# Performance work log

Measured on AMD Instinct MI355X. Metric: run time of the kernel, lower is better.

The kernel has to match this reference:

```python
import jax, jax.numpy as jnp
import numpy as np
from jax import lax

A_NUM = 3
STRIDES = (4, 8, 16, 32, 64)
LEVEL_HW = ((128, 208), (64, 104), (32, 52), (16, 26), (8, 13))
IMG_H, IMG_W = 512.0, 832.0
PRE_NMS, POST_NMS, NMS_TH = 6000, 1000, 0.7


def _base_anchors(base_size, ratios=(0.5, 1.0, 2.0), scales=(8.0,)):
    ratios = np.asarray(ratios, np.float64)
    scales = np.asarray(scales, np.float64)
    cx = cy = (base_size - 1) / 2.0
    size = float(base_size) * float(base_size)
    ws = np.round(np.sqrt(size / ratios))
    hs = np.round(ws * ratios)
    ws = (ws[:, None] * scales[None, :]).reshape(-1)
    hs = (hs[:, None] * scales[None, :]).reshape(-1)
    return np.stack([cx - 0.5 * (ws - 1), cy - 0.5 * (hs - 1),
                     cx + 0.5 * (ws - 1), cy + 0.5 * (hs - 1)], axis=1)


def _all_anchors():
    # generate_anchors_global: per-level shifted grids, concatenated, order (h, w, a)
    out = []
    for stride, (h, w) in zip(STRIDES, LEVEL_HW):
        base = _base_anchors(stride)  # [A,4]
        sx = np.arange(w) * stride
        sy = np.arange(h) * stride
        sx, sy = np.meshgrid(sx, sy)
        shifts = np.stack([sx.ravel(), sy.ravel(), sx.ravel(), sy.ravel()], axis=1)
        anc = (shifts[:, None, :] + base[None, :, :]).reshape(-1, 4)  # [H*W*A,4]
        out.append(anc)
    return np.concatenate(out, axis=0).astype(np.float32)

_ANCHORS = _all_anchors()


def _conv(x, w, b, pad):
    y = lax.conv_general_dilated(x, w, (1, 1), [(pad, pad), (pad, pad)],
                                 dimension_numbers=('NCHW', 'OIHW', 'NCHW'))
    return y + b[None, :, None, None]


def _bbox_transform_inv(anchors, deltas):
    w = anchors[:, 2] - anchors[:, 0] + 1.0
    h = anchors[:, 3] - anchors[:, 1] + 1.0
    cx = anchors[:, 0] + 0.5 * w
    cy = anchors[:, 1] + 0.5 * h
    dx, dy, dw, dh = deltas[:, 0], deltas[:, 1], deltas[:, 2], deltas[:, 3]
    pcx = dx * w + cx
    pcy = dy * h + cy
    pw = jnp.exp(dw) * w
    ph = jnp.exp(dh) * h
    return jnp.stack([pcx - 0.5 * pw, pcy - 0.5 * ph,
                      pcx + 0.5 * pw, pcy + 0.5 * ph], axis=1)


def _iou_one_to_many(box, boxes):
    area = (boxes[:, 2] - boxes[:, 0] + 1.0) * (boxes[:, 3] - boxes[:, 1] + 1.0)
    area_b = (box[2] - box[0] + 1.0) * (box[3] - box[1] + 1.0)
    xx1 = jnp.maximum(box[0], boxes[:, 0])
    yy1 = jnp.maximum(box[1], boxes[:, 1])
    xx2 = jnp.minimum(box[2], boxes[:, 2])
    yy2 = jnp.minimum(box[3], boxes[:, 3])
    iw = jnp.maximum(0.0, xx2 - xx1 + 1.0)
    ih = jnp.maximum(0.0, yy2 - yy1 + 1.0)
    inter = iw * ih
    return inter / (area + area_b - inter)


def _nms_fixed(boxes, scores, thresh, max_out):
    # greedy NMS with a fixed number of iterations (jit-friendly)
    def body(s, _):
        i = jnp.argmax(s)
        valid = s[i] > -jnp.inf
        ious = _iou_one_to_many(boxes[i], boxes)
        s2 = jnp.where(ious > thresh, -jnp.inf, s)
        s2 = s2.at[i].set(-jnp.inf)
        return s2, (i, valid)
    _, (idx, valid) = lax.scan(body, scores, None, length=max_out)
    return idx, valid


def _rpn_forward(feats, im_info, rpn_conv_w, rpn_conv_b, rpn_score_w,
                 rpn_score_b, rpn_bbox_w, rpn_bbox_b):
    fg_scores, bbox_deltas = [], []
    for p in feats:
        H, W = p.shape[-2], p.shape[-1]
        f = _conv(p, rpn_conv_w, rpn_conv_b, 1)              # [1,512,H,W]
        cls = _conv(f, rpn_score_w, rpn_score_b, 0)          # [1,2A,H,W]
        # _reshape_layer(.,2) + softmax(dim=1) + _reshape_layer back + permute
        prob = jax.nn.softmax(cls.reshape(1, 2, A_NUM, H, W), axis=1)
        prob = prob.reshape(1, 2 * A_NUM, H, W).transpose(0, 2, 3, 1)  # [1,H,W,2A]
        fg = prob[..., A_NUM:].reshape(-1)                    # fg prob, order (h,w,a)
        bb = _conv(f, rpn_bbox_w, rpn_bbox_b, 0).transpose(0, 2, 3, 1).reshape(-1, 4)
        fg_scores.append(fg)
        bbox_deltas.append(bb)
    scores = jnp.concatenate(fg_scores, axis=0)              # [Ntot]
    deltas = jnp.concatenate(bbox_deltas, axis=0)            # [Ntot,4]
    anchors = jnp.asarray(_ANCHORS)

    proposals = _bbox_transform_inv(anchors, deltas)
    # clip to image
    proposals = jnp.stack([
        jnp.clip(proposals[:, 0], 0.0, im_info[1] - 1.0),
        jnp.clip(proposals[:, 1], 0.0, im_info[0] - 1.0),
        jnp.clip(proposals[:, 2], 0.0, im_info[1] - 1.0),
        jnp.clip(proposals[:, 3], 0.0, im_info[0] - 1.0)], axis=1)

    # pre-NMS top-k by score
    top_scores, order = lax.top_k(scores, PRE_NMS)
    top_boxes = proposals[order]
    keep, valid = _nms_fixed(top_boxes, top_scores, NMS_TH, POST_NMS)
    vmask = valid.astype(top_boxes.dtype)[:, None]
    sel_boxes = top_boxes[keep] * vmask
    sel_scores = top_scores[keep][:, None] * vmask
    rois = jnp.concatenate([jnp.zeros((POST_NMS, 1), sel_boxes.dtype), sel_boxes], axis=1)
    return jnp.concatenate([rois, sel_scores], axis=1)        # [POST_NMS, 6]


def setup_inputs() -> dict:
    key = jax.random.key(0)
    ks = jax.random.split(key, 12)
    chans = 256
    feats = {}
    for i, (name, (h, w)) in enumerate(zip(['p2', 'p3', 'p4', 'p5', 'p6'], LEVEL_HW)):
        feats[name] = jax.random.normal(ks[i], (1, chans, h, w), jnp.float32)
    inp = dict(feats)
    inp['im_info'] = jnp.array([IMG_H, IMG_W, 1.0], jnp.float32)
    inp['rpn_conv_w'] = jax.random.normal(ks[5], (512, chans, 3, 3), jnp.float32) * 0.03
    inp['rpn_conv_b'] = jnp.zeros((512,), jnp.float32)
    inp['rpn_score_w'] = jax.random.normal(ks[6], (2 * A_NUM, 512, 1, 1), jnp.float32) * 0.03
    inp['rpn_score_b'] = jnp.zeros((2 * A_NUM,), jnp.float32)
    inp['rpn_bbox_w'] = jax.random.normal(ks[7], (4 * A_NUM, 512, 1, 1), jnp.float32) * 0.01
    inp['rpn_bbox_b'] = jnp.zeros((4 * A_NUM,), jnp.float32)
    return inp


def reference(p2, p3, p4, p5, p6, im_info, rpn_conv_w, rpn_conv_b,
              rpn_score_w, rpn_score_b, rpn_bbox_w, rpn_bbox_b):
    return _rpn_forward([p2, p3, p4, p5, p6], im_info, rpn_conv_w, rpn_conv_b,
                        rpn_score_w, rpn_score_b, rpn_bbox_w, rpn_bbox_b)
```

## Files before the change

### kernel.cpp

```cpp
#include <hip/hip_runtime.h>
#include <stdint.h>

#define N_ANCH   106392
#define PRE_NMS  6000
#define POST_NMS 1000
#define POOL_CAP 8192
#define NMS_BLKS 94
#define SUP_W    96

static __device__ const int    LV_H[5]      = {128, 64, 32, 16, 8};
static __device__ const int    LV_W[5]      = {208, 104, 52, 26, 13};
static __device__ const int    LV_STRIDE[5] = {4, 8, 16, 32, 64};
static __device__ const int    LV_PIX[5]    = {26624, 6656, 1664, 416, 104};
static __device__ const int    LV_TILE0[6]  = {0, 416, 520, 546, 553, 555};
static __device__ const int    LV_AOFF[6]   = {0, 79872, 99840, 104832, 106080, 106392};
static __device__ const int    GPOFF[6]     = {0, 26624, 33280, 34944, 35360, 35464};
static __device__ const double BASE_ANCH[5][3][4] = {
  {{-22.,-10.,25.,13.},   {-14.,-14.,17.,17.},    {-10.,-22.,13.,25.}},
  {{-40.,-20.,47.,27.},   {-28.,-28.,35.,35.},    {-20.,-44.,27.,51.}},
  {{-84.,-40.,99.,55.},   {-56.,-56.,71.,71.},    {-36.,-80.,51.,95.}},
  {{-164.,-72.,195.,103.},{-112.,-112.,143.,143.},{-76.,-168.,107.,199.}},
  {{-332.,-152.,395.,215.},{-224.,-224.,287.,287.},{-148.,-328.,211.,391.}}
};

__device__ __forceinline__ uint32_t sort32f(float f) {
  uint32_t u = __float_as_uint(f);
  return ((int)u < 0) ? ~u : (u | 0x80000000u);
}
__device__ __forceinline__ uint64_t sort64(double d) {
  uint64_t u = (uint64_t)__double_as_longlong(d);
  return ((long long)u < 0) ? ~u : (u | 0x8000000000000000ull);
}

__device__ __forceinline__ double combf(const float* sw, const float* bw, int c, int j) {
  if (j < 3) return (double)sw[(3 + j) * 512 + c] - (double)sw[j * 512 + c];
  return (double)bw[(j - 3) * 512 + c];
}

__global__ __launch_bounds__(256) void k_weff_part(const float* __restrict__ cw,
                                                   const float* __restrict__ sw,
                                                   const float* __restrict__ bw,
                                                   double* __restrict__ Wpart) {
  int chunk = blockIdx.x / 9;
  int tb = blockIdx.x % 9;
  int t = tb * 256 + threadIdx.x;
  int c0 = chunk * 32;
  double acc[15];
#pragma unroll
  for (int j = 0; j < 15; ++j) acc[j] = 0.0;
#pragma unroll 1
  for (int c = c0; c < c0 + 32; ++c) {
    double v = (double)cw[c * 2304 + t];
#pragma unroll
    for (int j = 0; j < 15; ++j) acc[j] += v * combf(sw, bw, c, j);
  }
  double* o = Wpart + (((size_t)chunk * 2304 + t) << 4);
#pragma unroll
  for (int j = 0; j < 15; ++j) o[j] = acc[j];
  o[15] = 0.0;
}

__global__ __launch_bounds__(256) void k_weff_fin(const double* __restrict__ Wpart,
                                                  const float* __restrict__ cb,
                                                  const float* __restrict__ sb,
                                                  const float* __restrict__ bb,
                                                  const float* __restrict__ sw,
                                                  const float* __restrict__ bw,
                                                  double* __restrict__ Weff,
                                                  double* __restrict__ fb,
                                                  float4* __restrict__ w3,
                                                  float* __restrict__ fb32) {
  if (blockIdx.x == 9) {
    __shared__ double ps[15][16];
    int tid = threadIdx.x;
    if (tid < 240) {
      int j = tid >> 4, part = tid & 15;
      double s = 0.0;
      for (int c = part * 32; c < part * 32 + 32; ++c)
        s += (double)cb[c] * combf(sw, bw, c, j);
      ps[j][part] = s;
    }
    __syncthreads();
    if (tid < 15) {
      double s = 0.0;
#pragma unroll
      for (int part = 0; part < 16; ++part) s += ps[tid][part];
      s += (tid < 3) ? ((double)sb[3 + tid] - (double)sb[tid]) : (double)bb[tid - 3];
      fb[tid] = s;
      if (tid < 3) fb32[tid] = (float)s;
    }
    if (tid == 15) fb32[3] = 0.f;
    return;
  }
  int t = blockIdx.x * 256 + threadIdx.x;
  double acc[15];
#pragma unroll
  for (int j = 0; j < 15; ++j) acc[j] = 0.0;
#pragma unroll 1
  for (int chunk = 0; chunk < 16; ++chunk) {
    const double* p = Wpart + (((size_t)chunk * 2304 + t) << 4);
#pragma unroll
    for (int j = 0; j < 15; ++j) acc[j] += p[j];
  }
  double* o = Weff + ((size_t)t << 4);
#pragma unroll
  for (int j = 0; j < 15; ++j) o[j] = acc[j];
  o[15] = 0.0;
  float4 wf;
  wf.x = (float)acc[0]; wf.y = (float)acc[1]; wf.z = (float)acc[2]; wf.w = 0.f;
  w3[t] = wf;
}

__global__ __launch_bounds__(256) void k_w5(const double* __restrict__ Weff,
                                            double* __restrict__ w5) {
  int idx = blockIdx.x * 256 + threadIdx.x;
  if (idx >= 2304 * 3) return;
  int t = idx / 3, a = idx % 3;
  int ci = t / 9, t9 = t % 9;
  const double* src = Weff + ((size_t)t << 4);
  double* dst = w5 + (size_t)ci * 192 + (size_t)(t9 * 3 + a) * 6;
  int jd = 3 + 4 * a;
  dst[0] = src[jd + 0];
  dst[1] = src[jd + 1];
  dst[2] = src[jd + 2];
  dst[3] = src[jd + 3];
  dst[4] = src[a];
  dst[5] = 0.0;
}

__device__ __forceinline__ void load9(float v[9], const float* __restrict__ ib,
                                      const bool rok[3], const bool cok[3],
                                      const int roff[3]) {
#pragma unroll
  for (int ky = 0; ky < 3; ++ky)
#pragma unroll
    for (int kx = 0; kx < 3; ++kx)
      v[ky * 3 + kx] = (rok[ky] && cok[kx]) ? ib[roff[ky] + kx] : 0.0f;
}

__global__ __launch_bounds__(256) void k_fast(
    const float* __restrict__ p0, const float* __restrict__ p1,
    const float* __restrict__ p2, const float* __restrict__ p3,
    const float* __restrict__ p4,
    const float4* __restrict__ w3, const float* __restrict__ fb32,
    float* __restrict__ logits32, uint32_t* __restrict__ hist) {
  __shared__ float4 w3s[2304];
  __shared__ float red[4][64][3];
  int tid = threadIdx.x, wv = tid >> 6, ln = tid & 63;
  for (int i = tid; i < 2304; i += 256) w3s[i] = w3[i];
  int t = blockIdx.x;
  int L = 0;
  while (L < 4 && t >= LV_TILE0[L + 1]) ++L;
  const float* inL = (L == 0) ? p0 : (L == 1) ? p1 : (L == 2) ? p2 : (L == 3) ? p3 : p4;
  int H = LV_H[L], W = LV_W[L], HW = H * W, PIX = LV_PIX[L];
  int pix = (t - LV_TILE0[L]) * 64 + ln;
  bool valid = pix < PIX;
  if (!valid) pix = PIX - 1;
  int h = pix / W, w = pix % W;
  bool rok[3], cok[3];
  int roff[3];
#pragma unroll
  for (int ky = 0; ky < 3; ++ky) {
    int iy = h + ky - 1;
    rok[ky] = (iy >= 0 && iy < H);
    roff[ky] = iy * W + w - 1;
  }
#pragma unroll
  for (int kx = 0; kx < 3; ++kx) {
    int ix = w + kx - 1;
    cok[kx] = (ix >= 0 && ix < W);
  }
  __syncthreads();
  float a0 = 0.f, a1 = 0.f, a2 = 0.f;
  int ci0 = wv * 64;
  const float* ib = inL + ci0 * HW;
#pragma unroll 1
  for (int ci = ci0; ci < ci0 + 64; ++ci, ib += HW) {
    float v[9];
    load9(v, ib, rok, cok, roff);
    const float4* wr = w3s + ci * 9;
#pragma unroll
    for (int t9 = 0; t9 < 9; ++t9) {
      float4 wt = wr[t9];
      float vv = v[t9];
      a0 += vv * wt.x; a1 += vv * wt.y; a2 += vv * wt.z;
    }
  }
  red[wv][ln][0] = a0; red[wv][ln][1] = a1; red[wv][ln][2] = a2;
  __syncthreads();
  if (wv == 0 && valid) {
    int gbase = LV_AOFF[L] + pix * 3;
#pragma unroll
    for (int a = 0; a < 3; ++a) {
      float f = (red[0][ln][a] + red[1][ln][a]) + (red[2][ln][a] + red[3][ln][a]);
      f += fb32[a];
      logits32[gbase + a] = f;
      atomicAdd(&hist[sort32f(f) >> 16], 1u);
    }
  }
}

__global__ __launch_bounds__(1024) void k_edge(const uint32_t* __restrict__ hist,
                                               uint32_t* __restrict__ cnts) {
  __shared__ uint32_t cs[1024];
  __shared__ uint32_t g_grp, g_suf;
  int t = threadIdx.x, wv = t >> 6, ln = t & 63;
#pragma unroll 4
  for (int r = 0; r < 64; ++r) {
    int g = r * 16 + wv;
    uint32_t x = hist[g * 64 + ln];
#pragma unroll
    for (int off = 32; off > 0; off >>= 1) x += __shfl_down(x, off);
    if (ln == 0) cs[g] = x;
  }
  __syncthreads();
  for (int off = 1; off < 1024; off <<= 1) {
    uint32_t v = cs[t] + ((t + off < 1024) ? cs[t + off] : 0u);
    __syncthreads();
    cs[t] = v;
    __syncthreads();
  }
  uint32_t sufnext = (t < 1023) ? cs[t + 1] : 0u;
  if (cs[t] >= PRE_NMS && sufnext < PRE_NMS) {
    g_grp = (uint32_t)t;
    g_suf = sufnext;
  }
  __syncthreads();
  if (t < 64) {
    uint32_t grp = g_grp, suf = g_suf;
    uint32_t x = hist[grp * 64 + t];
    uint32_t S = x;
#pragma unroll
    for (int off = 1; off < 64; off <<= 1) {
      uint32_t y = __shfl_down(S, off);
      if (t + off < 64) S += y;
    }
    unsigned long long mask = __ballot(suf + S >= PRE_NMS);
    int hi = 63 - (int)__clzll(mask);
    if (t == hi) {
      uint32_t e = grp * 64 + (uint32_t)hi;
      cnts[1] = (e > 2) ? e - 2 : 0;
    }
  }
}

__global__ __launch_bounds__(256) void k_cnt(const float* __restrict__ logits32,
                                             const uint32_t* __restrict__ cnts,
                                             uint32_t* __restrict__ bcnt) {
  __shared__ uint32_t wc[4];
  int tid = threadIdx.x;
  int i = blockIdx.x * 256 + tid;
  uint32_t edge = cnts[1];
  bool pass = (i < N_ANCH) && ((sort32f(logits32[i]) >> 16) >= edge);
  unsigned long long m = __ballot(pass);
  if ((tid & 63) == 0) wc[tid >> 6] = (uint32_t)__popcll(m);
  __syncthreads();
  if (tid == 0) bcnt[blockIdx.x] = wc[0] + wc[1] + wc[2] + wc[3];
}

__global__ __launch_bounds__(256) void k_fill(const float* __restrict__ logits32,
                                              uint32_t* __restrict__ cnts,
                                              const uint32_t* __restrict__ bcnt,
                                              uint32_t* __restrict__ alist) {
  __shared__ uint32_t red[256];
  __shared__ uint32_t woff[4];
  int tid = threadIdx.x, wv = tid >> 6, ln = tid & 63;
  uint32_t s = 0;
  for (int k = tid; k < blockIdx.x; k += 256) s += bcnt[k];
  red[tid] = s;
  __syncthreads();
#pragma unroll
  for (int off = 128; off > 0; off >>= 1) {
    if (tid < off) red[tid] += red[tid + off];
    __syncthreads();
  }
  uint32_t base = red[0];
  int i = blockIdx.x * 256 + tid;
  uint32_t edge = cnts[1];
  bool pass = (i < N_ANCH) && ((sort32f(logits32[i]) >> 16) >= edge);
  unsigned long long m = __ballot(pass);
  if (ln == 0) woff[wv] = (uint32_t)__popcll(m);
  __syncthreads();
  uint32_t off_in_blk = 0;
  for (int k = 0; k < wv; ++k) off_in_blk += woff[k];
  if (pass) {
    uint32_t pos = base + off_in_blk + (uint32_t)__popcll(m & ((1ull << ln) - 1ull));
    if (pos < POOL_CAP) alist[pos] = (uint32_t)i;
  }
  if (blockIdx.x == ((N_ANCH + 255) / 256 - 1) && tid == 0)
    cnts[0] = base + woff[0] + woff[1] + woff[2] + woff[3];
}

__global__ __launch_bounds__(256) void k_refine(
    const float* __restrict__ p0, const float* __restrict__ p1,
    const float* __restrict__ p2, const float* __restrict__ p3,
    const float* __restrict__ p4,
    const double* __restrict__ w5, const double* __restrict__ fb,
    const uint32_t* __restrict__ alist, const uint32_t* __restrict__ cnts,
    double* __restrict__ logits, double* __restrict__ deltas,
    uint64_t* __restrict__ pkey) {
  __shared__ int4 wlds[4][768];
  __shared__ double red[4][64][5];
  int tid = threadIdx.x, wv = tid >> 6, ln = tid & 63;
  int cnt = (int)cnts[0];
  if (cnt > POOL_CAP) cnt = POOL_CAP;
  int base = blockIdx.x * 64;
  if (base >= cnt) return;
  int slot = base + ln;
  if (slot >= cnt) slot = cnt - 1;
  int gi = (int)alist[slot];
  int gpix = gi / 3, a = gi - gpix * 3;
  int L = 0;
  while (L < 4 && gpix >= GPOFF[L + 1]) ++L;
  int pix = gpix - GPOFF[L];
  const float* inL = (L == 0) ? p0 : (L == 1) ? p1 : (L == 2) ? p2 : (L == 3) ? p3 : p4;
  int H = LV_H[L], W = LV_W[L], HW = H * W;
  int h = pix / W, w = pix % W;
  bool rok[3], cok[3];
  int roff[3];
#pragma unroll
  for (int ky = 0; ky < 3; ++ky) {
    int iy = h + ky - 1;
    rok[ky] = (iy >= 0 && iy < H);
    roff[ky] = iy * W + w - 1;
  }
#pragma unroll
  for (int kx = 0; kx < 3; ++kx) {
    int ix = w + kx - 1;
    cok[kx] = (ix >= 0 && ix < W);
  }
  const char* wbc = (const char*)&wlds[wv][0];
  {
    const int4* gs = (const int4*)((const char*)w5 + (size_t)(wv * 64) * 1536);
    int4 r[12];
#pragma unroll
    for (int i = 0; i < 12; ++i) r[i] = gs[i * 64 + ln];
#pragma unroll
    for (int i = 0; i < 12; ++i) wlds[wv][i * 64 + ln] = r[i];
  }
  double sc = 0.0, d0 = 0.0, d1 = 0.0, d2 = 0.0, d3 = 0.0;
  const float* ibn = inL + (size_t)(wv * 64) * HW;
  float vn[9];
  load9(vn, ibn, rok, cok, roff);
#pragma unroll 1
  for (int k = 0; k < 8; ++k) {
    int4 r[12];
    if (k < 7) {
      const int4* gs =
          (const int4*)((const char*)w5 + (size_t)(wv * 64 + (k + 1) * 8) * 1536);
#pragma unroll
      for (int i = 0; i < 12; ++i) r[i] = gs[i * 64 + ln];
    }
#pragma unroll 1
    for (int c2 = 0; c2 < 8; ++c2) {
      float vc[9];
#pragma unroll
      for (int q = 0; q < 9; ++q) vc[q] = vn[q];
      int lc = k * 8 + c2;
      if (lc < 63) {
        ibn += HW;
        load9(vn, ibn, rok, cok, roff);
      }
      const char* b2 = wbc + c2 * 1536 + a * 48;
#pragma unroll
      for (int t9 = 0; t9 < 9; ++t9) {
        double vd = (double)vc[t9];
        double2 w01 = *(const double2*)(b2 + t9 * 144);
        double2 w23 = *(const double2*)(b2 + t9 * 144 + 16);
        double  w4  = *(const double*)(b2 + t9 * 144 + 32);
        d0 += vd * w01.x; d1 += vd * w01.y;
        d2 += vd * w23.x; d3 += vd * w23.y;
        sc += vd * w4;
      }
    }
    if (k < 7) {
#pragma unroll
      for (int i = 0; i < 12; ++i) wlds[wv][i * 64 + ln] = r[i];
    }
  }
  red[wv][ln][0] = sc;
  red[wv][ln][1] = d0; red[wv][ln][2] = d1;
  red[wv][ln][3] = d2; red[wv][ln][4] = d3;
  __syncthreads();
  if (wv == 0) {
    int js = a, jd = 3 + 4 * a;
    double f[5];
#pragma unroll
    for (int j = 0; j < 5; ++j)
      f[j] = red[0][ln][j] + red[1][ln][j] + red[2][ln][j] + red[3][ln][j];
    double lg = f[0] + fb[js];
    logits[gi] = lg;
    deltas[gi * 4 + 0] = f[1] + fb[jd + 0];
    deltas[gi * 4 + 1] = f[2] + fb[jd + 1];
    deltas[gi * 4 + 2] = f[3] + fb[jd + 2];
    deltas[gi * 4 + 3] = f[4] + fb[jd + 3];
    pkey[slot] = (sort64(lg) & ~0x1FFFFull) | (uint64_t)(0x1FFFFu - (uint32_t)gi);
  }
}

__global__ __launch_bounds__(256) void k_rank_cnt(const uint32_t* __restrict__ cnts,
                                                  const uint64_t* __restrict__ pkey,
                                                  uint32_t* __restrict__ rank32) {
  __shared__ uint64_t lk[512];
  int t = threadIdx.x;
  int cnt = (int)cnts[0];
  if (cnt > POOL_CAP) cnt = POOL_CAP;
  int it = blockIdx.x >> 4, jc = blockIdx.x & 15;
  int e = it * 256 + t;
  int c0 = jc * 512;
  if (it * 256 >= cnt || c0 >= cnt) return;
  int lim = cnt - c0; if (lim > 512) lim = 512;
  for (int i = t; i < 512; i += 256) lk[i] = (i < lim) ? pkey[c0 + i] : 0ull;
  __syncthreads();
  bool active = e < cnt;
  uint64_t mykey = active ? pkey[e] : ~0ull;
  int r = 0;
#pragma unroll 8
  for (int j = 0; j < 512; ++j) r += (lk[j] > mykey) ? 1 : 0;
  if (active && r) atomicAdd(&rank32[e], (uint32_t)r);
}

__global__ __launch_bounds__(256) void k_scatter(const uint32_t* __restrict__ cnts,
                                                 const uint64_t* __restrict__ pkey,
                                                 const uint32_t* __restrict__ rank32,
                                                 const double* __restrict__ logits,
                                                 const double* __restrict__ deltas,
                                                 const float* __restrict__ im_info,
                                                 double* __restrict__ ss,
                                                 double* __restrict__ sbx,
                                                 float4* __restrict__ bxf,
                                                 float* __restrict__ areaf) {
  int t = threadIdx.x;
  int cnt = (int)cnts[0];
  if (cnt > POOL_CAP) cnt = POOL_CAP;
  int e = blockIdx.x * 256 + t;
  if (blockIdx.x * 256 >= cnt) return;
  if (e >= cnt) return;
  int rank = (int)rank32[e];
  if (rank >= PRE_NMS) return;
  uint64_t mykey = pkey[e];
  int gi = 0x1FFFF - (int)(mykey & 0x1FFFFull);
  int L = 0;
  while (L < 4 && gi >= LV_AOFF[L + 1]) ++L;
  int rel = gi - LV_AOFF[L];
  int pix = rel / 3, a = rel % 3;
  int W = LV_W[L];
  int h = pix / W, w = pix % W;
  double imW1 = (double)im_info[1] - 1.0;
  double imH1 = (double)im_info[0] - 1.0;
  double shx = (double)(w * LV_STRIDE[L]), shy = (double)(h * LV_STRIDE[L]);
  double ax1 = BASE_ANCH[L][a][0] + shx, ay1 = BASE_ANCH[L][a][1] + shy;
  double ax2 = BASE_ANCH[L][a][2] + shx, ay2 = BASE_ANCH[L][a][3] + shy;
  double dx = deltas[gi * 4 + 0], dy = deltas[gi * 4 + 1];
  double dw = deltas[gi * 4 + 2], dh = deltas[gi * 4 + 3];
  double wa = ax2 - ax1 + 1.0, ha = ay2 - ay1 + 1.0;
  double cx = ax1 + 0.5 * wa, cy = ay1 + 0.5 * ha;
  double pcx = dx * wa + cx, pcy = dy * ha + cy;
  double pw = exp(dw) * wa, ph = exp(dh) * ha;
  double x1 = fmin(fmax(pcx - 0.5 * pw, 0.0), imW1);
  double y1 = fmin(fmax(pcy - 0.5 * ph, 0.0), imH1);
  double x2 = fmin(fmax(pcx + 0.5 * pw, 0.0), imW1);
  double y2 = fmin(fmax(pcy + 0.5 * ph, 0.0), imH1);
  ss[rank] = 1.0 / (1.0 + exp(-logits[gi]));
  sbx[rank * 4 + 0] = x1; sbx[rank * 4 + 1] = y1;
  sbx[rank * 4 + 2] = x2; sbx[rank * 4 + 3] = y2;
  float4 bf;
  bf.x = (float)x1; bf.y = (float)y1; bf.z = (float)x2; bf.w = (float)y2;
  bxf[rank] = bf;
  areaf[rank] = (float)((x2 - x1 + 1.0) * (y2 - y1 + 1.0));
}

__device__ __forceinline__ bool iou_gt(const double* A, const double* B) {
  double areaA = (A[2] - A[0] + 1.0) * (A[3] - A[1] + 1.0);
  double areaB = (B[2] - B[0] + 1.0) * (B[3] - B[1] + 1.0);
  double xx1 = fmax(A[0], B[0]), yy1 = fmax(A[1], B[1]);
  double xx2 = fmin(A[2], B[2]), yy2 = fmin(A[3], B[3]);
  double iw = fmax(0.0, xx2 - xx1 + 1.0), ih = fmax(0.0, yy2 - yy1 + 1.0);
  double inter = iw * ih;
  return inter > 0.7 * (areaA + areaB - inter);
}

__global__ __launch_bounds__(256) void k_build(const double* __restrict__ sbx,
                                               const float4* __restrict__ bxf,
                                               const float* __restrict__ areaf,
                                               uint64_t* __restrict__ Sup) {
  __shared__ float cbx[256][5];
  __shared__ float rbx[64][5];
  int blk = blockIdx.x;
  int rtile = blk / 24, ctile = blk % 24;
  int t = threadIdx.x, q = t >> 6, ln = t & 63;
  int r = rtile * 64 + ln;
  int w = ctile * 4 + q;
  {
    int c = ctile * 256 + t;
    float4 b;
    float ar;
    if (c < NMS_BLKS * 64) { b = bxf[c]; ar = areaf[c]; }
    else { b.x = b.y = b.z = b.w = 0.f; ar = 0.f; }
    cbx[t][0] = b.x; cbx[t][1] = b.y; cbx[t][2] = b.z; cbx[t][3] = b.w; cbx[t][4] = ar;
    if (t < 64) {
      int rr = rtile * 64 + t;
      float4 rb = bxf[rr];
      rbx[t][0] = rb.x; rbx[t][1] = rb.y; rbx[t][2] = rb.z; rbx[t][3] = rb.w;
      rbx[t][4] = areaf[rr];
    }
  }
  __syncthreads();
  uint64_t bits = 0ull;
  int j0 = w * 64;
  if (w < NMS_BLKS && j0 + 63 > r) {
    float ax1 = rbx[ln][0], ay1 = rbx[ln][1], ax2 = rbx[ln][2], ay2 = rbx[ln][3];
    float aar = rbx[ln][4];
#pragma unroll 4
    for (int jj = 0; jj < 64; ++jj) {
      int j = j0 + jj;
      if (j <= r) continue;
      int cl = q * 64 + jj;
      float iw = fminf(ax2, cbx[cl][2]) - fmaxf(ax1, cbx[cl][0]) + 1.f;
      float ih = fminf(ay2, cbx[cl][3]) - fmaxf(ay1, cbx[cl][1]) + 1.f;
      float inter = fmaxf(iw, 0.f) * fmaxf(ih, 0.f);
      float d = inter - 0.7f * (aar + cbx[cl][4] - inter);
      bool sup;
      if (d > 4.0f) sup = true;
      else if (d < -4.0f) sup = false;
      else sup = iou_gt(sbx + (size_t)r * 4, sbx + (size_t)j * 4);
      if (sup) bits |= 1ull << jj;
    }
  }
  Sup[(size_t)r * SUP_W + w] = bits;
}

__global__ __launch_bounds__(1024) void k_scan(const uint64_t* __restrict__ Sup,
                                               const double* __restrict__ ss,
                                               const double* __restrict__ sbx,
                                               float* __restrict__ out) {
  __shared__ uint16_t keep[POST_NMS];
  __shared__ uint32_t ext_arr[SUP_W][2];
  __shared__ int s_kcnt, s_done;
  __shared__ int s_pend[2][2];
  int t = threadIdx.x, wv = t >> 6, ln = t & 63;
  for (int i = t; i < SUP_W * 2; i += 1024) ext_arr[i >> 1][i & 1] = 0u;
  if (t == 0) { s_kcnt = 0; s_done = 0; }
  if (t < 4) s_pend[t >> 1][t & 1] = 0;
  uint64_t diag = 0ull, nxt = 0ull;
  if (wv == 0) {
    size_t r = (size_t)ln * SUP_W;
    diag = Sup[r + 0];
    nxt  = Sup[r + 1];
  }
  __syncthreads();
  for (int b = 0; b < NMS_BLKS; ++b) {
    if (wv == 0) {
      uint64_t myrow = diag & ~((2ull << ln) - 1ull);
      uint64_t mynxt = nxt;
      if (b + 1 < NMS_BLKS) {
        size_t r = (size_t)((b + 1) * 64 + ln) * SUP_W;
        diag = Sup[r + (b + 1)];
        nxt  = Sup[r + (b + 2)];
      }
      uint64_t ext = ((uint64_t)ext_arr[b][1] << 32) | ext_arr[b][0];
      int base = b * 64;
      if (base + 63 >= PRE_NMS) {
        int v = PRE_NMS - base;
        ext |= ~((1ull << v) - 1ull);
      }
      int K0 = s_kcnt;
      uint64_t avail;
      {
        uint64_t a0 = ~ext;
        uint32_t alo = __builtin_amdgcn_readfirstlane((uint32_t)a0);
        uint32_t ahi = __builtin_amdgcn_readfirstlane((uint32_t)(a0 >> 32));
        avail = ((uint64_t)ahi << 32) | alo;
      }
      uint32_t mr_lo = (uint32_t)myrow, mr_hi = (uint32_t)(myrow >> 32);
      uint32_t mn_lo = (uint32_t)mynxt, mn_hi = (uint32_t)(mynxt >> 32);
      uint64_t kp = 0ull, extn = 0ull;
      int lim = POST_NMS - K0, nk = 0;
      while (avail && nk < lim) {
        int i2 = __ffsll((unsigned long long)avail) - 1;
        uint32_t rlo = (uint32_t)__builtin_amdgcn_readlane((int)mr_lo, i2);
        uint32_t rhi = (uint32_t)__builtin_amdgcn_readlane((int)mr_hi, i2);
        uint32_t qlo = (uint32_t)__builtin_amdgcn_readlane((int)mn_lo, i2);
        uint32_t qhi = (uint32_t)__builtin_amdgcn_readlane((int)mn_hi, i2);
        kp |= 1ull << i2;
        ++nk;
        extn |= ((uint64_t)qhi << 32) | qlo;
        avail &= ~(((uint64_t)rhi << 32) | rlo);
        avail &= ~(1ull << i2);
      }
      if ((kp >> ln) & 1ull) {
        int pos = K0 + __popcll(kp & ((1ull << ln) - 1ull));
        keep[pos] = (uint16_t)(base + ln);
      }
      if (ln == 0) {
        if ((uint32_t)extn)         atomicOr(&ext_arr[b + 1][0], (uint32_t)extn);
        if ((uint32_t)(extn >> 32)) atomicOr(&ext_arr[b + 1][1],
                                             (uint32_t)(extn >> 32));
        s_kcnt = K0 + nk;
        s_pend[(b + 1) & 1][0] = K0;
        s_pend[(b + 1) & 1][1] = K0 + nk;
        if (K0 + nk >= POST_NMS || b + 1 >= NMS_BLKS) s_done = 1;
      }
    } else {
      int lo = s_pend[b & 1][0], hi = s_pend[b & 1][1];
      if (hi > lo) {
        int tt = t - 64;
        int g = tt / 96, w = tt - g * 96;
        if (w >= b + 1) {
          uint64_t v = 0ull;
          for (int q = lo + g; q < hi; q += 10)
            v |= Sup[(size_t)keep[q] * SUP_W + w];
          if (v) {
            if ((uint32_t)v)         atomicOr(&ext_arr[w][0], (uint32_t)v);
            if ((uint32_t)(v >> 32)) atomicOr(&ext_arr[w][1], (uint32_t)(v >> 32));
          }
        }
      }
    }
    __syncthreads();
    if (s_done) break;
  }
  __syncthreads();
  int KF = s_kcnt;
  for (int r = t; r < POST_NMS; r += 1024) {
    float* o = out + r * 6;
    if (r < KF) {
      int p = keep[r];
      o[0] = 0.f;
      o[1] = (float)sbx[p * 4 + 0];
      o[2] = (float)sbx[p * 4 + 1];
      o[3] = (float)sbx[p * 4 + 2];
      o[4] = (float)sbx[p * 4 + 3];
      o[5] = (float)ss[p];
    } else {
#pragma unroll
      for (int c = 0; c < 6; ++c) o[c] = 0.f;
    }
  }
}

extern "C" void kernel_launch(void* const* d_in, const int* in_sizes, int n_in,
                              void* d_out, int out_size, void* d_ws, size_t ws_size,
                              hipStream_t stream) {
  const float* p0 = (const float*)d_in[0];
  const float* p1 = (const float*)d_in[1];
  const float* p2 = (const float*)d_in[2];
  const float* p3 = (const float*)d_in[3];
  const float* p4 = (const float*)d_in[4];
  const float* im_info = (const float*)d_in[5];
  const float* cw = (const float*)d_in[6];
  const float* cb = (const float*)d_in[7];
  const float* sw = (const float*)d_in[8];
  const float* sb = (const float*)d_in[9];
  const float* bw = (const float*)d_in[10];
  const float* bb = (const float*)d_in[11];
  char* ws = (char*)d_ws;
  uint32_t* hist    = (uint32_t*)(ws + 0);
  uint32_t* cnts    = (uint32_t*)(ws + 262144);
  double*   fb      = (double*)  (ws + 262208);
  float*    fb32    = (float*)   (ws + 262336);
  double*   logits  = (double*)  (ws + 262352);
  double*   deltas  = (double*)  (ws + 1113488);
  float*    logits32= (float*)   (ws + 4518032);
  float4*   w3      = (float4*)  (ws + 4943600);
  double*   Weff    = (double*)  (ws + 4980464);
  double*   Wpart   = (double*)  (ws + 5275376);
  uint32_t* alist   = (uint32_t*)(ws + 9993968);
  double*   ssort   = (double*)  (ws + 10026736);
  double*   sbx     = (double*)  (ws + 10074864);
  float4*   bxf     = (float4*)  (ws + 10267376);
  float*    areaf   = (float*)   (ws + 10363632);
  uint64_t* Sup     = (uint64_t*)(ws + 10387696);
  uint64_t* pkey    = (uint64_t*)(ws + 15007984);
  uint32_t* rank32  = (uint32_t*)(ws + 15073520);
  uint32_t* bcnt    = hist;
  double*   W5      = Wpart;
  float* out = (float*)d_out;

  hipMemsetAsync(ws, 0, 262208, stream);
  hipMemsetAsync(rank32, 0, 32768, stream);
  k_weff_part<<<144, 256, 0, stream>>>(cw, sw, bw, Wpart);
  k_weff_fin<<<10, 256, 0, stream>>>(Wpart, cb, sb, bb, sw, bw, Weff, fb, w3, fb32);
  k_w5<<<27, 256, 0, stream>>>(Weff, W5);
  k_fast<<<555, 256, 0, stream>>>(p0, p1, p2, p3, p4, w3, fb32, logits32, hist);
  k_edge<<<1, 1024, 0, stream>>>(hist, cnts);
  k_cnt<<<416, 256, 0, stream>>>(logits32, cnts, bcnt);
  k_fill<<<416, 256, 0, stream>>>(logits32, cnts, bcnt, alist);
  k_refine<<<128, 256, 0, stream>>>(p0, p1, p2, p3, p4, W5, fb, alist, cnts,
                                    logits, deltas, pkey);
  k_rank_cnt<<<512, 256, 0, stream>>>(cnts, pkey, rank32);
  k_scatter<<<32, 256, 0, stream>>>(cnts, pkey, rank32, logits, deltas, im_info,
                                    ssort, sbx, bxf, areaf);
  k_build<<<94 * 24, 256, 0, stream>>>(sbx, bxf, areaf, Sup);
  k_scan<<<1, 1024, 0, stream>>>(Sup, ssort, sbx, out);
}
```

Measured before the change: 436.4 us.

## Split refine kernel across more blocks with separate combine pass; prefetch k_fast inputs

k_refine now uses 128-thread blocks, twice as many, with each block handling half the input channels. Per-chunk partial sums go to a global buffer, and a new k_comb kernel reduces them and writes logits, deltas and sort keys. The aim is to spread the few refine blocks over more CUs. It costs an extra launch and global round trip, and the ppart buffer is placed inside an existing workspace region. k_fast also software-pipelines its 9-tap input loads one channel ahead.

Measured after the change: 415.6 us. 1.05x faster.

```diff
diff --git a/kernel.cpp b/kernel.cpp
--- a/kernel.cpp
+++ b/kernel.cpp
@@ -170,19 +170,26 @@
     int ix = w + kx - 1;
     cok[kx] = (ix >= 0 && ix < W);
   }
+  int ci0 = wv * 64;
+  const float* ibn = inL + ci0 * HW;
+  float vn[9];
+  load9(vn, ibn, rok, cok, roff);
   __syncthreads();
   float a0 = 0.f, a1 = 0.f, a2 = 0.f;
-  int ci0 = wv * 64;
-  const float* ib = inL + ci0 * HW;
 #pragma unroll 1
-  for (int ci = ci0; ci < ci0 + 64; ++ci, ib += HW) {
-    float v[9];
-    load9(v, ib, rok, cok, roff);
+  for (int ci = ci0; ci < ci0 + 64; ++ci) {
+    float vc[9];
+#pragma unroll
+    for (int q = 0; q < 9; ++q) vc[q] = vn[q];
+    if (ci < ci0 + 63) {
+      ibn += HW;
+      load9(vn, ibn, rok, cok, roff);
+    }
     const float4* wr = w3s + ci * 9;
 #pragma unroll
     for (int t9 = 0; t9 < 9; ++t9) {
       float4 wt = wr[t9];
-      float vv = v[t9];
+      float vv = vc[t9];
       a0 += vv * wt.x; a1 += vv * wt.y; a2 += vv * wt.z;
     }
   }
@@ -291,20 +298,19 @@
     cnts[0] = base + woff[0] + woff[1] + woff[2] + woff[3];
 }
 
-__global__ __launch_bounds__(256) void k_refine(
+__global__ __launch_bounds__(128) void k_refine(
     const float* __restrict__ p0, const float* __restrict__ p1,
     const float* __restrict__ p2, const float* __restrict__ p3,
     const float* __restrict__ p4,
-    const double* __restrict__ w5, const double* __restrict__ fb,
+    const double* __restrict__ w5,
     const uint32_t* __restrict__ alist, const uint32_t* __restrict__ cnts,
-    double* __restrict__ logits, double* __restrict__ deltas,
-    uint64_t* __restrict__ pkey) {
-  __shared__ int4 wlds[4][768];
-  __shared__ double red[4][64][5];
+    double* __restrict__ ppart) {
+  __shared__ int4 wlds[2][768];
   int tid = threadIdx.x, wv = tid >> 6, ln = tid & 63;
   int cnt = (int)cnts[0];
   if (cnt > POOL_CAP) cnt = POOL_CAP;
-  int base = blockIdx.x * 64;
+  int grp = blockIdx.x >> 1, half = blockIdx.x & 1;
+  int base = grp * 64;
   if (base >= cnt) return;
   int slot = base + ln;
   if (slot >= cnt) slot = cnt - 1;
@@ -329,9 +335,11 @@
     int ix = w + kx - 1;
     cok[kx] = (ix >= 0 && ix < W);
   }
+  int chunk = half * 2 + wv;
+  int ci0 = chunk * 64;
   const char* wbc = (const char*)&wlds[wv][0];
   {
-    const int4* gs = (const int4*)((const char*)w5 + (size_t)(wv * 64) * 1536);
+    const int4* gs = (const int4*)((const char*)w5 + (size_t)ci0 * 1536);
     int4 r[12];
 #pragma unroll
     for (int i = 0; i < 12; ++i) r[i] = gs[i * 64 + ln];
@@ -339,7 +347,7 @@
     for (int i = 0; i < 12; ++i) wlds[wv][i * 64 + ln] = r[i];
   }
   double sc = 0.0, d0 = 0.0, d1 = 0.0, d2 = 0.0, d3 = 0.0;
-  const float* ibn = inL + (size_t)(wv * 64) * HW;
+  const float* ibn = inL + (size_t)ci0 * HW;
   float vn[9];
   load9(vn, ibn, rok, cok, roff);
 #pragma unroll 1
@@ -347,7 +355,7 @@
     int4 r[12];
     if (k < 7) {
       const int4* gs =
-          (const int4*)((const char*)w5 + (size_t)(wv * 64 + (k + 1) * 8) * 1536);
+          (const int4*)((const char*)w5 + (size_t)(ci0 + (k + 1) * 8) * 1536);
 #pragma unroll
       for (int i = 0; i < 12; ++i) r[i] = gs[i * 64 + ln];
     }
@@ -378,24 +386,35 @@
       for (int i = 0; i < 12; ++i) wlds[wv][i * 64 + ln] = r[i];
     }
   }
-  red[wv][ln][0] = sc;
-  red[wv][ln][1] = d0; red[wv][ln][2] = d1;
-  red[wv][ln][3] = d2; red[wv][ln][4] = d3;
-  __syncthreads();
-  if (wv == 0) {
-    int js = a, jd = 3 + 4 * a;
-    double f[5];
-#pragma unroll
-    for (int j = 0; j < 5; ++j)
-      f[j] = red[0][ln][j] + red[1][ln][j] + red[2][ln][j] + red[3][ln][j];
-    double lg = f[0] + fb[js];
-    logits[gi] = lg;
-    deltas[gi * 4 + 0] = f[1] + fb[jd + 0];
-    deltas[gi * 4 + 1] = f[2] + fb[jd + 1];
-    deltas[gi * 4 + 2] = f[3] + fb[jd + 2];
-    deltas[gi * 4 + 3] = f[4] + fb[jd + 3];
-    pkey[slot] = (sort64(lg) & ~0x1FFFFull) | (uint64_t)(0x1FFFFu - (uint32_t)gi);
-  }
+  double* o = ppart + ((size_t)slot * 4 + chunk) * 5;
+  o[0] = sc; o[1] = d0; o[2] = d1; o[3] = d2; o[4] = d3;
+}
+
+__global__ __launch_bounds__(256) void k_comb(
+    const uint32_t* __restrict__ alist, const uint32_t* __restrict__ cnts,
+    const double* __restrict__ ppart, const double* __restrict__ fb,
+    double* __restrict__ logits, double* __restrict__ deltas,
+    uint64_t* __restrict__ pkey) {
+  int e = blockIdx.x * 256 + threadIdx.x;
+  int cnt = (int)cnts[0];
+  if (cnt > POOL_CAP) cnt = POOL_CAP;
+  if (blockIdx.x * 256 >= cnt) return;
+  if (e >= cnt) return;
+  int gi = (int)alist[e];
+  int a = gi - (gi / 3) * 3;
+  const double* p = ppart + (size_t)e * 20;
+  double f[5];
+#pragma unroll
+  for (int j = 0; j < 5; ++j)
+    f[j] = ((p[0 + j] + p[5 + j]) + p[10 + j]) + p[15 + j];
+  int js = a, jd = 3 + 4 * a;
+  double lg = f[0] + fb[js];
+  logits[gi] = lg;
+  deltas[gi * 4 + 0] = f[1] + fb[jd + 0];
+  deltas[gi * 4 + 1] = f[2] + fb[jd + 1];
+  deltas[gi * 4 + 2] = f[3] + fb[jd + 2];
+  deltas[gi * 4 + 3] = f[4] + fb[jd + 3];
+  pkey[e] = (sort64(lg) & ~0x1FFFFull) | (uint64_t)(0x1FFFFu - (uint32_t)gi);
 }
 
 __global__ __launch_bounds__(256) void k_rank_cnt(const uint32_t* __restrict__ cnts,
@@ -675,6 +694,7 @@
   uint32_t* rank32  = (uint32_t*)(ws + 15073520);
   uint32_t* bcnt    = hist;
   double*   W5      = Wpart;
+  double*   ppart   = (double*)(ws + 5275376 + 524288);
   float* out = (float*)d_out;
 
   hipMemsetAsync(ws, 0, 262208, stream);
@@ -686,8 +706,8 @@
   k_edge<<<1, 1024, 0, stream>>>(hist, cnts);
   k_cnt<<<416, 256, 0, stream>>>(logits32, cnts, bcnt);
   k_fill<<<416, 256, 0, stream>>>(logits32, cnts, bcnt, alist);
-  k_refine<<<128, 256, 0, stream>>>(p0, p1, p2, p3, p4, W5, fb, alist, cnts,
-                                    logits, deltas, pkey);
+  k_refine<<<256, 128, 0, stream>>>(p0, p1, p2, p3, p4, W5, alist, cnts, ppart);
+  k_comb<<<32, 256, 0, stream>>>(alist, cnts, ppart, fb, logits, deltas, pkey);
   k_rank_cnt<<<512, 256, 0, stream>>>(cnts, pkey, rank32);
   k_scatter<<<32, 256, 0, stream>>>(cnts, pkey, rank32, logits, deltas, im_info,
                                     ssort, sbx, bxf, areaf);
```
